# Kernel tuning notes

Hardware: AMD Instinct MI355X
Metric: run time of the kernel (lower is better)

The kernel has to match this reference:

```python
import jax, jax.numpy as jnp
import numpy as np

EMBED_DIM = 1024
NUM_HEADS = 16
HEAD_DIM = EMBED_DIM // NUM_HEADS
LORA_R = 128
LORA_SCALING = 1.0 / LORA_R  # loralib default lora_alpha=1


def setup_inputs() -> dict:
    key = jax.random.key(0)
    k1, k2, k3, k4 = jax.random.split(key, 4)
    B, S, E = 2, 2048, EMBED_DIM
    x = jax.random.normal(k1, (B, S, E), dtype=jnp.float32)
    # in_proj: LoRA linear 3E -> 3E (see notes), bias-free
    W_in = jax.random.normal(k2, (3 * E, 3 * E), dtype=jnp.float32) * (1.0 / np.sqrt(3 * E))
    A_in = jax.random.normal(k3, (LORA_R, 3 * E), dtype=jnp.float32) * (1.0 / np.sqrt(3 * E))
    B_in = jnp.zeros((3 * E, LORA_R), dtype=jnp.float32)  # loralib inits B to zero
    W_out = jax.random.normal(k4, (E, E), dtype=jnp.float32) * (1.0 / np.sqrt(E))
    return {"x": x, "W_in": W_in, "A_in": A_in, "B_in": B_in, "W_out": W_out}


def reference(x, W_in, A_in, B_in, W_out):
    B, S, E = x.shape
    H, D = NUM_HEADS, HEAD_DIM
    x3 = jnp.concatenate([x, x, x], axis=-1)  # [B,S,3E]
    # LoRA linear: x3 @ W^T + (x3 @ A^T) @ B^T * scaling
    qkv = x3 @ W_in.T + ((x3 @ A_in.T) @ B_in.T) * LORA_SCALING  # [B,S,3E]
    Q, K, V = jnp.split(qkv, 3, axis=-1)
    # [B,S,E] -> [B,H,S,D]
    Q = Q.reshape(B, S, H, D).transpose(0, 2, 1, 3)
    K = K.reshape(B, S, H, D).transpose(0, 2, 1, 3)
    V = V.reshape(B, S, H, D).transpose(0, 2, 1, 3)
    scores = jnp.einsum("bhqd,bhkd->bhqk", Q, K) / jnp.sqrt(jnp.float32(D))
    attn = jax.nn.softmax(scores, axis=-1)
    out = jnp.einsum("bhqk,bhkd->bhqd", attn, V)  # [B,H,S,D]
    out = out.transpose(0, 2, 1, 3).reshape(B, S, E)
    return out @ W_out.T
```

## Files before the change

### kernel.cpp

```cpp
#include <hip/hip_runtime.h>

#define E_DIM 1024
#define H_NUM 16
#define D_HEAD 64
#define SEQ 2048
#define BATCH 2
#define NTOK 4096
#define R_LORA 128
#define Q3 3072

#if __has_builtin(__builtin_amdgcn_exp2f)
#define K_PRESCALE (0.125f * 1.44269504088896f)
#define FAST_EXP(x) __builtin_amdgcn_exp2f(x)
#else
#define K_PRESCALE 0.125f
#define FAST_EXP(x) __expf(x)
#endif

typedef float floatx4 __attribute__((ext_vector_type(4)));
typedef __bf16 bf16x8 __attribute__((ext_vector_type(8)));
typedef __bf16 bf16x4 __attribute__((ext_vector_type(4)));
typedef bf16x8 bf16x8_al __attribute__((may_alias));
typedef bf16x4 bf16x4_al __attribute__((may_alias));

__device__ __forceinline__ void async_cp16(const void* g, void* l) {
  __builtin_amdgcn_global_load_lds(
      (__attribute__((address_space(1))) unsigned int*)(size_t)g,
      (__attribute__((address_space(3))) unsigned int*)l, 16, 0, 0);
}

__device__ __forceinline__ void wg_barrier() {
  asm volatile("" ::: "memory");
  __builtin_amdgcn_s_barrier();
  asm volatile("" ::: "memory");
}

__global__ __launch_bounds__(256) void prep_all(const float* __restrict__ x,
                                                const float* __restrict__ Wi,
                                                const float* __restrict__ Bl,
                                                const float* __restrict__ Ai,
                                                const float* __restrict__ Wo,
                                                __bf16* __restrict__ xb,
                                                __bf16* __restrict__ wtot,
                                                __bf16* __restrict__ binb,
                                                __bf16* __restrict__ aeffT,
                                                __bf16* __restrict__ wob) {
  __shared__ __bf16 tile[64][65];
  const int blk = blockIdx.x, t = threadIdx.x;
  if (blk < 4096) {
    int idx = (blk * 256 + t) * 4;
    float4 v = *(const float4*)(x + idx);
    bf16x4 o = {(__bf16)v.x, (__bf16)v.y, (__bf16)v.z, (__bf16)v.w};
    *(bf16x4_al*)(xb + idx) = o;
  } else if (blk < 7168) {
    int j = blk - 4096, e = t * 4;
    const float* r = Wi + (size_t)j * Q3;
    float4 a = *(const float4*)(r + e);
    float4 b = *(const float4*)(r + e + 1024);
    float4 c = *(const float4*)(r + e + 2048);
    bf16x4 o = {(__bf16)(a.x + b.x + c.x), (__bf16)(a.y + b.y + c.y),
                (__bf16)(a.z + b.z + c.z), (__bf16)(a.w + b.w + c.w)};
    *(bf16x4_al*)(wtot + (size_t)j * E_DIM + e) = o;
  } else if (blk < 7552) {
    int idx = (blk - 7168) * 256 + t;
    int j = idx >> 5, cq = (idx & 31) * 4;
    float4 v = *(const float4*)(Bl + (size_t)j * R_LORA + cq);
    bf16x4 o = {(__bf16)v.x, (__bf16)v.y, (__bf16)v.z, (__bf16)v.w};
    *(bf16x4_al*)(binb + (size_t)j * R_LORA + cq) = o;
  } else if (blk < 7584) {
    int b2 = blk - 7552;
    int r0 = (b2 & 1) * 64, e0 = (b2 >> 1) * 64;
    int c = t & 63, r4 = t >> 6;
#pragma unroll
    for (int i = 0; i < 16; i++) {
      int row = r4 + i * 4;
      const float* rp = Ai + (size_t)(r0 + row) * Q3 + e0 + c;
      tile[row][c] = (__bf16)(rp[0] + rp[1024] + rp[2048]);
    }
    __syncthreads();
#pragma unroll
    for (int i = 0; i < 16; i++) {
      int er = r4 + i * 4;
      aeffT[(size_t)(e0 + er) * R_LORA + r0 + c] = tile[c][er];
    }
  } else {
    int idx = ((blk - 7584) * 256 + t) * 4;
    float4 v = *(const float4*)(Wo + idx);
    bf16x4 o = {(__bf16)v.x, (__bf16)v.y, (__bf16)v.z, (__bf16)v.w};
    *(bf16x4_al*)(wob + idx) = o;
  }
}

template <int KTOT, int LDA, int LDB, int EPI>
__global__ __launch_bounds__(256) void gemm_mfma(const __bf16* A, const __bf16* Bm,
                                                 float* fOut, __bf16* o0, __bf16* o1,
                                                 __bf16* o2) {
  __shared__ __bf16 lds[8192];
  const int t = threadIdx.x;
  const int wave = t >> 6, lane = t & 63;
  const int wm = wave & 1, wn = wave >> 1;
  const int lr = lane & 15, lq = lane >> 4;
  const int m0 = blockIdx.x * 128, n0 = blockIdx.y * 128;

  floatx4 acc[4][4] = {};
  const __bf16* gA = A + (size_t)(m0 + lr) * LDA + lq * 8;
  const __bf16* gB = Bm + (size_t)(n0 + lr) * LDB + lq * 8;

  for (int kk = 0; kk < KTOT; kk += 32) {
    __syncthreads();
    async_cp16(gA + (size_t)(wave * 16) * LDA + kk, lds + wave * 512);
    async_cp16(gA + (size_t)((wave + 4) * 16) * LDA + kk, lds + (wave + 4) * 512);
    async_cp16(gB + (size_t)(wave * 16) * LDB + kk, lds + 4096 + wave * 512);
    async_cp16(gB + (size_t)((wave + 4) * 16) * LDB + kk, lds + 4096 + (wave + 4) * 512);
    __syncthreads();
    bf16x8 af[4], bfr[4];
#pragma unroll
    for (int i = 0; i < 4; i++)
      af[i] = *(const bf16x8_al*)(lds + (wm * 4 + i) * 512 + lane * 8);
#pragma unroll
    for (int j = 0; j < 4; j++)
      bfr[j] = *(const bf16x8_al*)(lds + 4096 + (wn * 4 + j) * 512 + lane * 8);
#pragma unroll
    for (int i = 0; i < 4; i++)
#pragma unroll
      for (int j = 0; j < 4; j++)
        acc[i][j] = __builtin_amdgcn_mfma_f32_16x16x32_bf16(af[i], bfr[j], acc[i][j], 0, 0, 0);
  }

#pragma unroll
  for (int i = 0; i < 4; i++)
#pragma unroll
    for (int j = 0; j < 4; j++) {
      const int row0 = m0 + wm * 64 + i * 16 + lq * 4;
      const int col = n0 + wn * 64 + j * 16 + lr;
      if (EPI == 0) {
#pragma unroll
        for (int r = 0; r < 4; r++)
          fOut[(size_t)(row0 + r) * 1024 + col] = acc[i][j][r];
      } else if (EPI == 3) {
#pragma unroll
        for (int r = 0; r < 4; r++) {
          size_t off = (size_t)(row0 + r) * 1024 + col;
          o0[off] = (__bf16)((float)o0[off] + acc[i][j][r] * (1.0f / 128.0f));
        }
      } else {
        int part = col >> 10, e = col & 1023, h = e >> 6, d = e & 63;
        int b = row0 >> 11, s = row0 & 2047;
        if (part == 2) {
          bf16x4 pv;
#pragma unroll
          for (int r = 0; r < 4; r++) pv[r] = (__bf16)acc[i][j][r];
          *(bf16x4_al*)(o2 + ((size_t)(b * H_NUM + h) * D_HEAD + d) * SEQ + s) = pv;
        } else {
#pragma unroll
          for (int r = 0; r < 4; r++) {
            float v = acc[i][j][r];
            if (part == 1) v *= K_PRESCALE;
            size_t off = ((size_t)(b * H_NUM + h) * SEQ + (s + r)) * D_HEAD + d;
            (part == 0 ? o0 : o1)[off] = (__bf16)v;
          }
        }
      }
    }
}

__global__ __launch_bounds__(256, 2) void attn_kernel(const __bf16* __restrict__ Q,
                                                      const __bf16* __restrict__ K,
                                                      const __bf16* __restrict__ Vt,
                                                      __bf16* __restrict__ O) {
  __shared__ __bf16 smem[40960];
  const int t = threadIdx.x, wave = t >> 6, lane = t & 63;
  const int lr = lane & 15, lq = lane >> 4;
  const int lin = blockIdx.x;
  const int xcd = lin & 7, ix = lin >> 3;
  const int bh = xcd * 4 + (ix >> 4);
  const int q0 = (ix & 15) * 128;
  __bf16* plsw = smem + 32768 + wave * 2048;
  const size_t hbase = (size_t)bh * SEQ * D_HEAD;
  const __bf16* Kp = K + hbase;
  const __bf16* vtb = Vt + (size_t)bh * D_HEAD * SEQ;
  const int row7 = lr & 7;

  bf16x8 qf[2][2];
#pragma unroll
  for (int qg = 0; qg < 2; qg++) {
    const __bf16* qp = Q + hbase + (size_t)(q0 + wave * 32 + qg * 16 + lr) * D_HEAD + lq * 8;
    qf[qg][0] = *(const bf16x8_al*)qp;
    qf[qg][1] = *(const bf16x8_al*)(qp + 32);
  }
  asm volatile("" : "+v"(qf[0][0]), "+v"(qf[0][1]), "+v"(qf[1][0]), "+v"(qf[1][1]));

  floatx4 oacc[2][4] = {};
  float lsum[2] = {0.0f, 0.0f};

  auto STAGE = [&](int ktb, int bb) {
#pragma unroll
    for (int ii = 0; ii < 8; ii++) {
      int sg = wave * 8 + ii;
      const __bf16* src;
      if (sg < 16) {
        src = Kp + (size_t)(ktb + (sg >> 1) * 16 + lr) * D_HEAD + (sg & 1) * 32 + lq * 8;
      } else {
        int v = sg - 16;
        src = vtb + (size_t)((v >> 2) * 16 + lr) * SEQ + ktb + (v & 3) * 32 + lq * 8;
      }
      async_cp16(src, smem + bb + sg * 512);
    }
  };

  STAGE(0, 0);

  const int NT = SEQ / 128;
  for (int it = 0; it < NT; ++it) {
    const int cur = (it & 1) ? 16384 : 0;
    wg_barrier();
    if (it + 1 < NT) {
      STAGE((it + 1) * 128, 16384 - cur);
      asm volatile("s_waitcnt vmcnt(8)" ::: "memory");
    } else {
      asm volatile("s_waitcnt vmcnt(0)" ::: "memory");
    }
    wg_barrier();
    const __bf16* kls = smem + cur;
    const __bf16* vls = smem + cur + 8192;

#pragma unroll
    for (int h = 0; h < 2; h++) {
#pragma unroll
      for (int kb = 0; kb < 4; kb++) {
        bf16x8 kf0 = *(const bf16x8_al*)(kls + (h * 8 + kb * 2) * 512 + lane * 8);
        bf16x8 kf1 = *(const bf16x8_al*)(kls + (h * 8 + kb * 2 + 1) * 512 + lane * 8);
#pragma unroll
        for (int qg = 0; qg < 2; qg++) {
          floatx4 sv = {};
          __builtin_amdgcn_s_setprio(1);
          sv = __builtin_amdgcn_mfma_f32_16x16x32_bf16(kf0, qf[qg][0], sv, 0, 0, 0);
          sv = __builtin_amdgcn_mfma_f32_16x16x32_bf16(kf1, qf[qg][1], sv, 0, 0, 0);
          __builtin_amdgcn_s_setprio(0);
          bf16x4 pv;
#pragma unroll
          for (int r = 0; r < 4; r++) {
            float p = FAST_EXP(sv[r]);
            lsum[qg] += p;
            pv[r] = (__bf16)p;
          }
          int chunk = (kb * 2 + (lq >> 1)) ^ row7;
          *(bf16x4_al*)(plsw + qg * 1024 + lr * 64 + chunk * 8 + (lq & 1) * 4) = pv;
        }
      }

#pragma unroll
      for (int kc = 0; kc < 2; kc++) {
        bf16x8 vf[4];
#pragma unroll
        for (int jd = 0; jd < 4; jd++)
          vf[jd] = *(const bf16x8_al*)(vls + (jd * 4 + h * 2 + kc) * 512 + lane * 8);
        int chunk = (kc * 4 + lq) ^ row7;
#pragma unroll
        for (int qg = 0; qg < 2; qg++) {
          bf16x8 pf = *(const bf16x8_al*)(plsw + qg * 1024 + lr * 64 + chunk * 8);
          __builtin_amdgcn_s_setprio(1);
#pragma unroll
          for (int jd = 0; jd < 4; jd++)
            oacc[qg][jd] = __builtin_amdgcn_mfma_f32_16x16x32_bf16(pf, vf[jd], oacc[qg][jd], 0, 0, 0);
          __builtin_amdgcn_s_setprio(0);
        }
      }
    }
  }

#pragma unroll
  for (int qg = 0; qg < 2; qg++) {
    lsum[qg] += __shfl_xor(lsum[qg], 16);
    lsum[qg] += __shfl_xor(lsum[qg], 32);
  }

  const int b = bh >> 4, hh = bh & 15;
#pragma unroll
  for (int qg = 0; qg < 2; qg++)
#pragma unroll
    for (int r = 0; r < 4; r++) {
      float linv = 1.0f / __shfl(lsum[qg], lq * 4 + r);
      int s = q0 + wave * 32 + qg * 16 + lq * 4 + r;
#pragma unroll
      for (int jd = 0; jd < 4; jd++) {
        int d = jd * 16 + lr;
        O[((size_t)b * SEQ + s) * E_DIM + hh * D_HEAD + d] = (__bf16)(oacc[qg][jd][r] * linv);
      }
    }
}

extern "C" void kernel_launch(void* const* d_in, const int* in_sizes, int n_in,
                              void* d_out, int out_size, void* d_ws, size_t ws_size,
                              hipStream_t stream) {
  const float* x  = (const float*)d_in[0];
  const float* Wi = (const float*)d_in[1];
  const float* Ai = (const float*)d_in[2];
  const float* Bi = (const float*)d_in[3];
  const float* Wo = (const float*)d_in[4];
  float* out = (float*)d_out;
  char* ws = (char*)d_ws;

  __bf16* xb    = (__bf16*)(ws);
  __bf16* wtot  = (__bf16*)(ws + 8388608);
  __bf16* binb  = (__bf16*)(ws + 14680064);
  __bf16* aeffT = (__bf16*)(ws + 15466496);
  __bf16* wob   = (__bf16*)(ws + 15728640);
  __bf16* qh    = (__bf16*)(ws + 17825792);
  __bf16* kh    = (__bf16*)(ws + 26214400);
  __bf16* vt    = (__bf16*)(ws + 34603008);
  __bf16* oh    = (__bf16*)(ws + 42991616);

  prep_all<<<8608, 256, 0, stream>>>(x, Wi, Bi, Ai, Wo, xb, wtot, binb, aeffT, wob);

  gemm_mfma<128, 128, 128, 3><<<dim3(24, 8), 256, 0, stream>>>(
      binb, aeffT, nullptr, wtot, nullptr, nullptr);
  gemm_mfma<1024, 1024, 1024, 1><<<dim3(32, 24), 256, 0, stream>>>(
      xb, wtot, nullptr, qh, kh, vt);
  attn_kernel<<<dim3(512), 256, 0, stream>>>(qh, kh, vt, oh);
  gemm_mfma<1024, 1024, 1024, 0><<<dim3(32, 8), 256, 0, stream>>>(
      oh, wob, out, nullptr, nullptr, nullptr);
}
```

Baseline: 233.4 us.

## Triple-buffer LDS tiles in MFMA GEMM with async prefetch two stages ahead

Expands the GEMM shared-memory buffer to three stages and issues async global-to-LDS copies two k-steps ahead, waiting with explicit vmcnt counts instead of a full sync before each compute step. This is meant to hide global memory latency behind MFMA work. It triples LDS use per block, which may reduce occupancy, and it relies on correct vmcnt accounting and on the wg_barrier helper.

```diff
diff --git a/kernel.cpp b/kernel.cpp
--- a/kernel.cpp
+++ b/kernel.cpp
@@ -95,7 +95,7 @@
 __global__ __launch_bounds__(256) void gemm_mfma(const __bf16* A, const __bf16* Bm,
                                                  float* fOut, __bf16* o0, __bf16* o1,
                                                  __bf16* o2) {
-  __shared__ __bf16 lds[8192];
+  __shared__ __bf16 lds[24576];
   const int t = threadIdx.x;
   const int wave = t >> 6, lane = t & 63;
   const int wm = wave & 1, wn = wave >> 1;
@@ -106,25 +106,43 @@
   const __bf16* gA = A + (size_t)(m0 + lr) * LDA + lq * 8;
   const __bf16* gB = Bm + (size_t)(n0 + lr) * LDB + lq * 8;
 
+  auto STAGE = [&](int kk, int bb) {
+    async_cp16(gA + (size_t)(wave * 16) * LDA + kk, lds + bb + wave * 512);
+    async_cp16(gA + (size_t)((wave + 4) * 16) * LDA + kk, lds + bb + (wave + 4) * 512);
+    async_cp16(gB + (size_t)(wave * 16) * LDB + kk, lds + bb + 4096 + wave * 512);
+    async_cp16(gB + (size_t)((wave + 4) * 16) * LDB + kk, lds + bb + 4096 + (wave + 4) * 512);
+  };
+
+  STAGE(0, 0);
+  STAGE(32, 8192);
+  int cur = 0, tgt = 16384;
+
   for (int kk = 0; kk < KTOT; kk += 32) {
-    __syncthreads();
-    async_cp16(gA + (size_t)(wave * 16) * LDA + kk, lds + wave * 512);
-    async_cp16(gA + (size_t)((wave + 4) * 16) * LDA + kk, lds + (wave + 4) * 512);
-    async_cp16(gB + (size_t)(wave * 16) * LDB + kk, lds + 4096 + wave * 512);
-    async_cp16(gB + (size_t)((wave + 4) * 16) * LDB + kk, lds + 4096 + (wave + 4) * 512);
-    __syncthreads();
+    wg_barrier();
+    if (kk + 64 < KTOT) {
+      STAGE(kk + 64, tgt);
+      asm volatile("s_waitcnt vmcnt(8)" ::: "memory");
+    } else if (kk + 32 < KTOT) {
+      asm volatile("s_waitcnt vmcnt(4)" ::: "memory");
+    } else {
+      asm volatile("s_waitcnt vmcnt(0)" ::: "memory");
+    }
+    wg_barrier();
+    const int cb = cur;
     bf16x8 af[4], bfr[4];
 #pragma unroll
     for (int i = 0; i < 4; i++)
-      af[i] = *(const bf16x8_al*)(lds + (wm * 4 + i) * 512 + lane * 8);
+      af[i] = *(const bf16x8_al*)(lds + cb + (wm * 4 + i) * 512 + lane * 8);
 #pragma unroll
     for (int j = 0; j < 4; j++)
-      bfr[j] = *(const bf16x8_al*)(lds + 4096 + (wn * 4 + j) * 512 + lane * 8);
+      bfr[j] = *(const bf16x8_al*)(lds + cb + 4096 + (wn * 4 + j) * 512 + lane * 8);
 #pragma unroll
     for (int i = 0; i < 4; i++)
 #pragma unroll
       for (int j = 0; j < 4; j++)
         acc[i][j] = __builtin_amdgcn_mfma_f32_16x16x32_bf16(af[i], bfr[j], acc[i][j], 0, 0, 0);
+    cur += 8192; if (cur == 24576) cur = 0;
+    tgt += 8192; if (tgt == 24576) tgt = 0;
   }
 
 #pragma unroll
```

Result: faster. 220.1 us (-5.7%).
